# Kernel tuning notes

Measured on AMD Instinct MI355X. Metric: run time of the kernel, lower is better.

The kernel has to match this reference:

```python
import jax, jax.numpy as jnp
import numpy as np

MARGIN = 0.3


def setup_inputs() -> dict:
    key = jax.random.key(0)
    k1, k2 = jax.random.split(key)
    B, D, NCLS = 4096, 2048, 64
    inputs = jax.random.normal(k1, (B, D), dtype=jnp.float32)
    targets = jax.random.randint(k2, (B,), 0, NCLS, dtype=jnp.int64)
    return {"inputs": inputs, "targets": targets}


def _triplet_loss(inputs, targets, margin):
    sq = jnp.sum(inputs * inputs, axis=1)  # [B]
    distmat = sq[:, None] + sq[None, :] - 2.0 * (inputs @ inputs.T)  # [B, B]
    distmat = jnp.sqrt(jnp.clip(distmat, 1e-12, None))
    same = targets[None, :] == targets[:, None]  # [B, B]; includes diagonal
    neg_inf = jnp.float32(-jnp.inf)
    pos_inf = jnp.float32(jnp.inf)
    d_pos = jnp.max(jnp.where(same, distmat, neg_inf), axis=1)  # hardest positive
    d_neg = jnp.min(jnp.where(same, pos_inf, distmat), axis=1)  # hardest negative
    # MarginRankingLoss(x1=d_neg, x2=d_pos, y=1): mean(relu(-(d_neg - d_pos) + margin))
    return jnp.mean(jax.nn.relu(d_pos - d_neg + margin))


def reference(inputs, targets):
    return _triplet_loss(inputs, targets, MARGIN)
```

## Files before the change

kernel.cpp:

```cpp
#include <hip/hip_runtime.h>
#include <hip/hip_bf16.h>


typedef __attribute__((ext_vector_type(8))) short short8;
typedef __attribute__((ext_vector_type(4))) float f32x4;
using bf16 = __hip_bfloat16;

#define BN_ROWS 4096
#define D_DIM   2048
#define TILE    128
#define BK      64
#define NSTEP   (D_DIM / BK)
#define NB      (BN_ROWS / TILE)
#define NBLK    (NB * (NB + 1) / 2)
#define MARGIN  0.3f

__device__ __forceinline__ void gload16(const bf16* g, bf16* l) {
  __builtin_amdgcn_global_load_lds(
      (const __attribute__((address_space(1))) void*)g,
      (__attribute__((address_space(3))) void*)l, 16, 0, 0);
}

__global__ __launch_bounds__(256) void prep_kernel(
    const float* __restrict__ x, bf16* __restrict__ xb, float* __restrict__ sqv,
    unsigned* __restrict__ pos, unsigned* __restrict__ neg) {
  const int row = blockIdx.x;
  const int t = threadIdx.x;
  const float4* xr = (const float4*)(x + (size_t)row * D_DIM);
  bf16* xbr = xb + (size_t)row * D_DIM;
  float s = 0.f;
  #pragma unroll
  for (int p = 0; p < 2; ++p) {
    const int idx = t + p * 256;
    float4 a = xr[idx];
    s += a.x * a.x + a.y * a.y + a.z * a.z + a.w * a.w;
    union { ushort4 v; bf16 h[4]; } u;
    u.h[0] = __float2bfloat16(a.x);
    u.h[1] = __float2bfloat16(a.y);
    u.h[2] = __float2bfloat16(a.z);
    u.h[3] = __float2bfloat16(a.w);
    *(ushort4*)(xbr + (size_t)idx * 4) = u.v;
  }
  #pragma unroll
  for (int o = 32; o; o >>= 1) s += __shfl_down(s, o, 64);
  __shared__ float red[4];
  if ((t & 63) == 0) red[t >> 6] = s;
  __syncthreads();
  if (t == 0) {
    sqv[row] = red[0] + red[1] + red[2] + red[3];
    pos[row] = 0u;
    neg[row] = 0x7F800000u;
  }
}

__global__ __launch_bounds__(256) void gram_kernel(
    const bf16* __restrict__ xb, const float* __restrict__ sqv,
    const int* __restrict__ tgt, unsigned* __restrict__ pos,
    unsigned* __restrict__ neg) {
  __shared__ bf16 As[2][TILE * BK];
  __shared__ bf16 Bs[2][TILE * BK];
  const int t = threadIdx.x;
  const int wave = t >> 6, lane = t & 63;

  const int id = (blockIdx.x & 7) * (NBLK / 8) + (blockIdx.x >> 3);

  int by = (int)(0.5f * (65.0f - sqrtf(4225.0f - 8.0f * (float)id)));
  while (by * NB - (by * (by - 1)) / 2 > id) --by;
  while ((by + 1) * NB - ((by + 1) * by) / 2 <= id) ++by;
  const int bx = by + (id - (by * NB - (by * (by - 1)) / 2));
  const int rowBase = by * TILE;
  const int colBase = bx * TILE;

  const int wr = wave >> 1, wc = wave & 1;
  const int lhi = lane >> 4, llo = lane & 15;

  f32x4 acc[4][4];
  #pragma unroll
  for (int m = 0; m < 4; ++m)
    #pragma unroll
    for (int n = 0; n < 4; ++n) acc[m][n] = (f32x4){0.f, 0.f, 0.f, 0.f};

  const int srow = lane >> 3;
  const int swz = (lane & 7) ^ srow;

  auto stage = [&](int buf, int step) {
    const size_t kcol = (size_t)step * BK + (size_t)swz * 8;
    #pragma unroll
    for (int c = 0; c < 4; ++c) {
      const int chunk = wave * 4 + c;
      gload16(xb + (size_t)(rowBase + chunk * 8 + srow) * D_DIM + kcol,
              &As[buf][chunk * 512]);
      gload16(xb + (size_t)(colBase + chunk * 8 + srow) * D_DIM + kcol,
              &Bs[buf][chunk * 512]);
    }
  };

  auto compute = [&](int buf) {
    #pragma unroll
    for (int kk = 0; kk < 2; ++kk) {
      short8 af[4], bfr[4];
      #pragma unroll
      for (int m = 0; m < 4; ++m) {
        const int row = wr * 64 + m * 16 + llo;
        const int c16 = (kk * 4 + lhi) ^ (row & 7);
        af[m] = *(const short8*)(&As[buf][row * 64 + c16 * 8]);
      }
      #pragma unroll
      for (int n = 0; n < 4; ++n) {
        const int row = wc * 64 + n * 16 + llo;
        const int c16 = (kk * 4 + lhi) ^ (row & 7);
        bfr[n] = *(const short8*)(&Bs[buf][row * 64 + c16 * 8]);
      }
      #pragma unroll
      for (int m = 0; m < 4; ++m)
        #pragma unroll
        for (int n = 0; n < 4; ++n)
          acc[m][n] = __builtin_amdgcn_mfma_f32_16x16x32_bf16(
              af[m], bfr[n], acc[m][n], 0, 0, 0);
    }
  };

  stage(0, 0);
  __syncthreads();
  for (int step = 0; step < NSTEP - 1; ++step) {
    const int cur = step & 1;
    stage(cur ^ 1, step + 1);
    compute(cur);
    __syncthreads();
  }
  compute((NSTEP - 1) & 1);

  const float inf = __uint_as_float(0x7F800000u);
  float sqj[4];
  int tgj[4];
  #pragma unroll
  for (int n = 0; n < 4; ++n) {
    const int j = colBase + wc * 64 + n * 16 + llo;
    sqj[n] = sqv[j];
    tgj[n] = tgt[j];
  }
  float colP[4] = {0.f, 0.f, 0.f, 0.f};
  float colN[4] = {inf, inf, inf, inf};

  #pragma unroll
  for (int m = 0; m < 4; ++m) {
    #pragma unroll
    for (int r = 0; r < 4; ++r) {
      const int i = rowBase + wr * 64 + m * 16 + lhi * 4 + r;
      const float sqi = sqv[i];
      const int tgi = tgt[i];
      float pm = 0.0f, nm = inf;
      #pragma unroll
      for (int n = 0; n < 4; ++n) {
        const float g = acc[m][n][r];
        const float d2 = sqi + sqj[n] - 2.0f * g;
        const float d = sqrtf(fmaxf(d2, 1e-12f));
        if (tgj[n] == tgi) {
          pm = fmaxf(pm, d);
          colP[n] = fmaxf(colP[n], d);
        } else {
          nm = fminf(nm, d);
          colN[n] = fminf(colN[n], d);
        }
      }
      #pragma unroll
      for (int o = 1; o < 16; o <<= 1) {
        pm = fmaxf(pm, __shfl_xor(pm, o, 64));
        nm = fminf(nm, __shfl_xor(nm, o, 64));
      }
      if (llo == 0) {
        atomicMax(pos + i, __float_as_uint(pm));
        atomicMin(neg + i, __float_as_uint(nm));
      }
    }
  }
  #pragma unroll
  for (int n = 0; n < 4; ++n) {
    float cp = colP[n], cn = colN[n];
    cp = fmaxf(cp, __shfl_xor(cp, 16, 64));
    cp = fmaxf(cp, __shfl_xor(cp, 32, 64));
    cn = fminf(cn, __shfl_xor(cn, 16, 64));
    cn = fminf(cn, __shfl_xor(cn, 32, 64));
    if (lane < 16) {
      const int j = colBase + wc * 64 + n * 16 + llo;
      atomicMax(pos + j, __float_as_uint(cp));
      atomicMin(neg + j, __float_as_uint(cn));
    }
  }
}

__global__ __launch_bounds__(1024) void loss_kernel(
    const unsigned* __restrict__ pos, const unsigned* __restrict__ neg,
    float* __restrict__ out) {
  const int t = threadIdx.x;
  float s = 0.f;
  for (int i = t; i < BN_ROWS; i += 1024) {
    const float dp = __uint_as_float(pos[i]);
    const float dn = __uint_as_float(neg[i]);
    const float v = dp - dn + MARGIN;
    s += v > 0.f ? v : 0.f;
  }
  #pragma unroll
  for (int o = 32; o; o >>= 1) s += __shfl_down(s, o, 64);
  __shared__ float red[16];
  if ((t & 63) == 0) red[t >> 6] = s;
  __syncthreads();
  if (t < 16) {
    float v = red[t];
    #pragma unroll
    for (int o = 8; o; o >>= 1) v += __shfl_down(v, o, 16);
    if (t == 0) out[0] = v * (1.0f / (float)BN_ROWS);
  }
}

extern "C" void kernel_launch(void* const* d_in, const int* in_sizes, int n_in,
                              void* d_out, int out_size, void* d_ws, size_t ws_size,
                              hipStream_t stream) {
  const float* x = (const float*)d_in[0];
  const int* tgt = (const int*)d_in[1];
  float* out = (float*)d_out;

  char* ws = (char*)d_ws;
  bf16* xb = (bf16*)ws;
  float* sqv = (float*)(ws + (size_t)BN_ROWS * D_DIM * 2);
  unsigned* pos = (unsigned*)((char*)sqv + BN_ROWS * 4);
  unsigned* neg = (unsigned*)((char*)pos + BN_ROWS * 4);

  prep_kernel<<<BN_ROWS, 256, 0, stream>>>(x, xb, sqv, pos, neg);
  gram_kernel<<<NBLK, 256, 0, stream>>>(xb, sqv, tgt, pos, neg);
  loss_kernel<<<1, 1024, 0, stream>>>(pos, neg, out);
}
```

Baseline: 173.9 us.

## Load A fragments directly from global into registers, keep only B in LDS

The gram kernel stops staging the A tile in shared memory. Each wave now owns 32 full rows, loads its A fragments straight from global memory into registers (double-buffered across steps), and reads the whole 128-column B tile from LDS. The wave layout moves from 2x2 to 4x1, so each wave holds 2x8 MFMA tiles, and launch bounds ask for 2 blocks per CU. The aim is to halve LDS footprint and LDS read traffic. The cost is unswizzled, less coalesced global reads for A, higher register pressure, and A loads whose latency is exposed to the MFMA loop.

```diff
diff --git a/kernel.cpp b/kernel.cpp
--- a/kernel.cpp
+++ b/kernel.cpp
@@ -53,11 +53,10 @@
   }
 }
 
-__global__ __launch_bounds__(256) void gram_kernel(
+__global__ __launch_bounds__(256, 2) void gram_kernel(
     const bf16* __restrict__ xb, const float* __restrict__ sqv,
     const int* __restrict__ tgt, unsigned* __restrict__ pos,
     unsigned* __restrict__ neg) {
-  __shared__ bf16 As[2][TILE * BK];
   __shared__ bf16 Bs[2][TILE * BK];
   const int t = threadIdx.x;
   const int wave = t >> 6, lane = t & 63;
@@ -71,87 +70,96 @@
   const int rowBase = by * TILE;
   const int colBase = bx * TILE;
 
-  const int wr = wave >> 1, wc = wave & 1;
   const int lhi = lane >> 4, llo = lane & 15;
 
-  f32x4 acc[4][4];
-  #pragma unroll
-  for (int m = 0; m < 4; ++m)
-    #pragma unroll
-    for (int n = 0; n < 4; ++n) acc[m][n] = (f32x4){0.f, 0.f, 0.f, 0.f};
+  f32x4 acc[2][8];
+  #pragma unroll
+  for (int m = 0; m < 2; ++m)
+    #pragma unroll
+    for (int n = 0; n < 8; ++n) acc[m][n] = (f32x4){0.f, 0.f, 0.f, 0.f};
 
   const int srow = lane >> 3;
   const int swz = (lane & 7) ^ srow;
 
-  auto stage = [&](int buf, int step) {
+  auto stageB = [&](int buf, int step) {
     const size_t kcol = (size_t)step * BK + (size_t)swz * 8;
     #pragma unroll
     for (int c = 0; c < 4; ++c) {
       const int chunk = wave * 4 + c;
-      gload16(xb + (size_t)(rowBase + chunk * 8 + srow) * D_DIM + kcol,
-              &As[buf][chunk * 512]);
       gload16(xb + (size_t)(colBase + chunk * 8 + srow) * D_DIM + kcol,
               &Bs[buf][chunk * 512]);
     }
   };
 
-  auto compute = [&](int buf) {
+  auto loadA = [&](int step, short8* af) {
+    const size_t kc = (size_t)step * BK;
+    #pragma unroll
+    for (int kk = 0; kk < 2; ++kk)
+      #pragma unroll
+      for (int m = 0; m < 2; ++m) {
+        const int row = rowBase + wave * 32 + m * 16 + llo;
+        af[kk * 2 + m] = *(const short8*)(
+            xb + (size_t)row * D_DIM + kc + (size_t)(kk * 32 + lhi * 8));
+      }
+  };
+
+  auto computeS = [&](const short8* af, int buf) {
     #pragma unroll
     for (int kk = 0; kk < 2; ++kk) {
-      short8 af[4], bfr[4];
-      #pragma unroll
-      for (int m = 0; m < 4; ++m) {
-        const int row = wr * 64 + m * 16 + llo;
-        const int c16 = (kk * 4 + lhi) ^ (row & 7);
-        af[m] = *(const short8*)(&As[buf][row * 64 + c16 * 8]);
-      }
-      #pragma unroll
-      for (int n = 0; n < 4; ++n) {
-        const int row = wc * 64 + n * 16 + llo;
+      short8 bfr[8];
+      #pragma unroll
+      for (int n = 0; n < 8; ++n) {
+        const int row = n * 16 + llo;
         const int c16 = (kk * 4 + lhi) ^ (row & 7);
         bfr[n] = *(const short8*)(&Bs[buf][row * 64 + c16 * 8]);
       }
       #pragma unroll
-      for (int m = 0; m < 4; ++m)
+      for (int m = 0; m < 2; ++m)
         #pragma unroll
-        for (int n = 0; n < 4; ++n)
+        for (int n = 0; n < 8; ++n)
           acc[m][n] = __builtin_amdgcn_mfma_f32_16x16x32_bf16(
-              af[m], bfr[n], acc[m][n], 0, 0, 0);
+              af[kk * 2 + m], bfr[n], acc[m][n], 0, 0, 0);
     }
   };
 
-  stage(0, 0);
+  short8 afA[4], afB[4];
+  stageB(0, 0);
+  loadA(0, afA);
   __syncthreads();
-  for (int step = 0; step < NSTEP - 1; ++step) {
-    const int cur = step & 1;
-    stage(cur ^ 1, step + 1);
-    compute(cur);
+  for (int s = 0; s < NSTEP; s += 2) {
+    if (s + 1 < NSTEP) { loadA(s + 1, afB); stageB(1, s + 1); }
+    computeS(afA, 0);
     __syncthreads();
-  }
-  compute((NSTEP - 1) & 1);
+    if (s + 2 < NSTEP) { loadA(s + 2, afA); stageB(0, s + 2); }
+    if (s + 1 < NSTEP) {
+      computeS(afB, 1);
+      __syncthreads();
+    }
+  }
 
   const float inf = __uint_as_float(0x7F800000u);
-  float sqj[4];
-  int tgj[4];
-  #pragma unroll
-  for (int n = 0; n < 4; ++n) {
-    const int j = colBase + wc * 64 + n * 16 + llo;
+  float sqj[8];
+  int tgj[8];
+  #pragma unroll
+  for (int n = 0; n < 8; ++n) {
+    const int j = colBase + n * 16 + llo;
     sqj[n] = sqv[j];
     tgj[n] = tgt[j];
   }
-  float colP[4] = {0.f, 0.f, 0.f, 0.f};
-  float colN[4] = {inf, inf, inf, inf};
-
-  #pragma unroll
-  for (int m = 0; m < 4; ++m) {
+  float colP[8], colN[8];
+  #pragma unroll
+  for (int n = 0; n < 8; ++n) { colP[n] = 0.f; colN[n] = inf; }
+
+  #pragma unroll
+  for (int m = 0; m < 2; ++m) {
     #pragma unroll
     for (int r = 0; r < 4; ++r) {
-      const int i = rowBase + wr * 64 + m * 16 + lhi * 4 + r;
+      const int i = rowBase + wave * 32 + m * 16 + lhi * 4 + r;
       const float sqi = sqv[i];
       const int tgi = tgt[i];
       float pm = 0.0f, nm = inf;
       #pragma unroll
-      for (int n = 0; n < 4; ++n) {
+      for (int n = 0; n < 8; ++n) {
         const float g = acc[m][n][r];
         const float d2 = sqi + sqj[n] - 2.0f * g;
         const float d = sqrtf(fmaxf(d2, 1e-12f));
@@ -175,14 +183,14 @@
     }
   }
   #pragma unroll
-  for (int n = 0; n < 4; ++n) {
+  for (int n = 0; n < 8; ++n) {
     float cp = colP[n], cn = colN[n];
     cp = fmaxf(cp, __shfl_xor(cp, 16, 64));
     cp = fmaxf(cp, __shfl_xor(cp, 32, 64));
     cn = fminf(cn, __shfl_xor(cn, 16, 64));
     cn = fminf(cn, __shfl_xor(cn, 32, 64));
     if (lane < 16) {
-      const int j = colBase + wc * 64 + n * 16 + llo;
+      const int j = colBase + n * 16 + llo;
       atomicMax(pos + j, __float_as_uint(cp));
       atomicMin(neg + j, __float_as_uint(cn));
     }
```

New measurement: 168.9 us. 1.03x faster.
